# Kernel tuning notes

Hardware: AMD Instinct MI355X
Metric: run time of the kernel (lower is better)

The kernel has to match this reference:

```python
import jax, jax.numpy as jnp
import numpy as np

N = 100000       # nodes
DEG = 16         # fixed out/in degree used to build CSR
E = N * DEG      # edges
D_IN = 128       # in_feats
D_OUT = 256      # out_feats
K = 32           # maxk k_value


def _xavier_uniform(key, shape, gain):
    fan_out, fan_in = shape
    bound = gain * np.sqrt(6.0 / (fan_in + fan_out))
    return jax.random.uniform(key, shape, jnp.float32, -bound, bound)


def setup_inputs() -> dict:
    key = jax.random.key(0)
    ks = jax.random.split(key, 6)
    feat = jax.random.normal(ks[0], (N, D_IN), jnp.float32)
    topk_values = jax.random.uniform(ks[1], (N, K), jnp.float32)
    topk_indices = jax.random.randint(ks[2], (N, K), 0, D_IN).astype(jnp.int32)
    # CSR graph: fixed degree -> indptr is arange*DEG; random destinations
    indptr = (jnp.arange(N + 1) * DEG).astype(jnp.int32)
    indices = jax.random.randint(ks[3], (E,), 0, N).astype(jnp.int32)
    # set_graph_data: csr weight[e] = 1 / clamp(in_degree(dst), 1)
    in_deg = jax.ops.segment_sum(jnp.ones(E, jnp.float32), indices, num_segments=N)
    in_deg = jnp.maximum(in_deg, 1.0)
    csr_values = 1.0 / in_deg[indices]
    gain = np.sqrt(2.0)  # calculate_gain('relu')
    w_neigh = _xavier_uniform(ks[4], (D_OUT, D_IN), gain)
    w_self = _xavier_uniform(ks[5], (D_OUT, D_IN), gain)
    b_self = jnp.zeros((D_OUT,), jnp.float32)
    return {"feat": feat, "topk_values": topk_values, "csr_values": csr_values,
            "w_neigh": w_neigh, "w_self": w_self, "b_self": b_self,
            "topk_indices": topk_indices, "indptr": indptr, "indices": indices}


def reference(feat, topk_values, csr_values, w_neigh, w_self, b_self,
              topk_indices, indptr, indices):
    # Densify the k-sparse MaxK features: x[n, topk_indices[n, j]] = topk_values[n, j]
    x = jnp.zeros((N, D_IN), feat.dtype).at[
        jnp.arange(N)[:, None], topk_indices].add(topk_values)
    # Edge-weight-normalized SpMM over CSR: out[row] += w[e] * x[col[e]]
    row_ids = jnp.repeat(jnp.arange(N), jnp.diff(indptr), total_repeat_length=E)
    msgs = x[indices] * csr_values[:, None]          # [E, D_IN]
    agg = jax.ops.segment_sum(msgs, row_ids, num_segments=N)  # [N, D_IN]
    # lin_before_mp is False (in_feats <= out_feats): project after aggregation
    h_neigh = agg @ w_neigh.T                        # [N, D_OUT]
    rst = feat @ w_self.T + b_self + h_neigh         # fc_self(h_self) + h_neigh
    return rst
```

## Files before the change

kernel.cpp:

```cpp
#include <hip/hip_runtime.h>
#include <hip/hip_bf16.h>
#include <stdint.h>

#define N_NODES 100000
#define DEG 16
#define D_IN 128
#define D_OUT 256
#define K_TOP 32
#define K_CAT 256

typedef __attribute__((ext_vector_type(8))) short short8;
typedef __attribute__((ext_vector_type(4))) float floatx4;

__device__ __forceinline__ unsigned pack_bf16_rne(float f) {
    union { float f; unsigned u; } c; c.f = f;
    unsigned u = c.u;
    return (u + 0x7fffu + ((u >> 16) & 1u)) >> 16;
}
__device__ __forceinline__ float bf16lo_to_f(unsigned lo16) {
    union { unsigned u; float f; } c; c.u = lo16 << 16; return c.f;
}

__global__ __launch_bounds__(256) void k_packw(const float* __restrict__ w_self,
                                               const float* __restrict__ w_neigh,
                                               unsigned short* __restrict__ bmat) {
    int o = blockIdx.x;
    int k = threadIdx.x;
    float v = (k < D_IN) ? w_self[o * D_IN + k] : w_neigh[o * D_IN + (k - D_IN)];
    bmat[o * K_CAT + k] = (unsigned short)pack_bf16_rne(v);
}

#define DROWS 64
__global__ __launch_bounds__(256) void k_densify(const float* __restrict__ topk_v,
                                                 const int* __restrict__ topk_i,
                                                 const float* __restrict__ feat,
                                                 unsigned short* __restrict__ xbf,
                                                 unsigned short* __restrict__ abf) {
    __shared__ float sx[DROWS * D_IN];
    const int t = threadIdx.x;
    const int row0 = blockIdx.x * DROWS;

    #pragma unroll
    for (int p = 0; p < 8; ++p)
        *(floatx4*)&sx[(t + p * 256) * 4] = (floatx4){0.f, 0.f, 0.f, 0.f};
    __syncthreads();

    const size_t tbase = (size_t)row0 * K_TOP;
    #pragma unroll
    for (int p = 0; p < 8; ++p) {
        int q = t + p * 256;
        int r = q >> 5;
        if (row0 + r < N_NODES) {
            int   ci = topk_i[tbase + q];
            float cv = topk_v[tbase + q];
            atomicAdd(&sx[r * D_IN + ci], cv);
        }
    }
    __syncthreads();

    #pragma unroll
    for (int p = 0; p < 16; ++p) {
        int d = t + p * 256;
        int r = d >> 6;
        int c2 = (d & 63) * 2;
        if (row0 + r < N_NODES) {
            float2 v = *(const float2*)&sx[r * D_IN + c2];
            ((unsigned*)(xbf + (size_t)(row0 + r) * D_IN))[d & 63] =
                pack_bf16_rne(v.x) | (pack_bf16_rne(v.y) << 16);
        }
    }

    #pragma unroll
    for (int p = 0; p < 8; ++p) {
        int q = t + p * 256;
        int r = q >> 5;
        int c4 = (q & 31) * 4;
        if (row0 + r < N_NODES) {
            float4 f = *(const float4*)(feat + (size_t)(row0 + r) * D_IN + c4);
            uint2 pk;
            pk.x = pack_bf16_rne(f.x) | (pack_bf16_rne(f.y) << 16);
            pk.y = pack_bf16_rne(f.z) | (pack_bf16_rne(f.w) << 16);
            ((uint2*)(abf + (size_t)(row0 + r) * K_CAT))[q & 31] = pk;
        }
    }
}

__global__ __launch_bounds__(256) void k_spmm(const float* __restrict__ csr_w,
                                              const int* __restrict__ col_idx,
                                              const unsigned short* __restrict__ xbf,
                                              unsigned short* __restrict__ abf) {
    const int wave = threadIdx.x >> 6;
    const int lane = threadIdx.x & 63;
    const int pair = blockIdx.x * 4 + wave;
    const int row  = 2 * pair + (lane >> 5);
    const int hl   = lane & 31;
    if (row >= N_NODES) return;

    int c = 0; float w = 0.f;
    if (hl < DEG) {
        c = col_idx[row * DEG + hl];
        w = csr_w[row * DEG + hl];
    }
    const int bsel = lane & 32;
    uint2 vv[DEG];
    #pragma unroll
    for (int e = 0; e < DEG; ++e) {
        int col = __shfl(c, bsel | e);
        vv[e] = *(const uint2*)(xbf + (size_t)col * D_IN + hl * 4);
    }
    float a0 = 0.f, a1 = 0.f, a2 = 0.f, a3 = 0.f;
    #pragma unroll
    for (int e = 0; e < DEG; ++e) {
        float we = __shfl(w, bsel | e);
        a0 += we * bf16lo_to_f(vv[e].x & 0xffffu);
        a1 += we * bf16lo_to_f(vv[e].x >> 16);
        a2 += we * bf16lo_to_f(vv[e].y & 0xffffu);
        a3 += we * bf16lo_to_f(vv[e].y >> 16);
    }
    uint2 pk;
    pk.x = pack_bf16_rne(a0) | (pack_bf16_rne(a1) << 16);
    pk.y = pack_bf16_rne(a2) | (pack_bf16_rne(a3) << 16);
    ((uint2*)(abf + (size_t)row * K_CAT + D_IN))[hl] = pk;
}

#define BM 128
#define BN 256
#define BK 32
#define LDP 40

__global__ __launch_bounds__(256, 2) void k_gemm(const unsigned short* __restrict__ abf,
                                                 const unsigned short* __restrict__ bmat,
                                                 const float* __restrict__ bias,
                                                 float* __restrict__ out) {
    __shared__ unsigned short As[BM * LDP];
    __shared__ unsigned short Bs[BN * LDP];
    int t = threadIdx.x;
    int lane = t & 63, wave = t >> 6;
    int wr = wave >> 1, wc = wave & 1;
    int row0 = blockIdx.x * BM;

    floatx4 acc[4][8];
    #pragma unroll
    for (int i = 0; i < 4; ++i)
        #pragma unroll
        for (int j = 0; j < 8; ++j)
            acc[i][j] = (floatx4){0.f, 0.f, 0.f, 0.f};

    int quad = lane >> 4;
    int l16  = lane & 15;

    for (int kt = 0; kt < K_CAT; kt += BK) {
        __syncthreads();
        #pragma unroll
        for (int p = 0; p < 2; ++p) {
            int chunk = t + p * 256;
            int r  = chunk >> 2;
            int ko = (chunk & 3) * 8;
            uint4 av = make_uint4(0u, 0u, 0u, 0u);
            int gr = row0 + r;
            if (gr < N_NODES)
                av = *(const uint4*)(abf + (size_t)gr * K_CAT + kt + ko);
            *(uint4*)&As[r * LDP + ko] = av;
        }
        #pragma unroll
        for (int p = 0; p < 4; ++p) {
            int chunk = t + p * 256;
            int r  = chunk >> 2;
            int ko = (chunk & 3) * 8;
            uint4 bv = *(const uint4*)(bmat + (size_t)r * K_CAT + kt + ko);
            *(uint4*)&Bs[r * LDP + ko] = bv;
        }
        __syncthreads();

        short8 afr[4], bfr[8];
        #pragma unroll
        for (int i = 0; i < 4; ++i) {
            int m = wr * 64 + i * 16 + l16;
            afr[i] = *(const short8*)&As[m * LDP + quad * 8];
        }
        #pragma unroll
        for (int j = 0; j < 8; ++j) {
            int n = wc * 128 + j * 16 + l16;
            bfr[j] = *(const short8*)&Bs[n * LDP + quad * 8];
        }
        #pragma unroll
        for (int i = 0; i < 4; ++i)
            #pragma unroll
            for (int j = 0; j < 8; ++j)
                acc[i][j] = __builtin_amdgcn_mfma_f32_16x16x32_bf16(afr[i], bfr[j], acc[i][j], 0, 0, 0);
    }

    #pragma unroll
    for (int j = 0; j < 8; ++j) {
        int cg = wc * 128 + j * 16 + l16;
        float bv = bias[cg];
        #pragma unroll
        for (int i = 0; i < 4; ++i) {
            int mbase = row0 + wr * 64 + i * 16 + quad * 4;
            #pragma unroll
            for (int r = 0; r < 4; ++r) {
                int gr = mbase + r;
                if (gr < N_NODES) out[(size_t)gr * D_OUT + cg] = acc[i][j][r] + bv;
            }
        }
    }
}

extern "C" void kernel_launch(void* const* d_in, const int* in_sizes, int n_in,
                              void* d_out, int out_size, void* d_ws, size_t ws_size,
                              hipStream_t stream) {
    const float* feat    = (const float*)d_in[0];
    const float* topk_v  = (const float*)d_in[1];
    const float* csr_w   = (const float*)d_in[2];
    const float* w_neigh = (const float*)d_in[3];
    const float* w_self  = (const float*)d_in[4];
    const float* b_self  = (const float*)d_in[5];
    const int*   topk_i  = (const int*)d_in[6];
    const int*   indices = (const int*)d_in[8];
    float* out = (float*)d_out;

    unsigned short* xbf  = (unsigned short*)d_ws;
    unsigned short* abf  = xbf + (size_t)N_NODES * D_IN;
    unsigned short* bmat = abf + (size_t)N_NODES * K_CAT;

    k_packw<<<dim3(256), dim3(256), 0, stream>>>(w_self, w_neigh, bmat);
    k_densify<<<dim3((N_NODES + DROWS - 1) / DROWS), dim3(256), 0, stream>>>(topk_v, topk_i, feat, xbf, abf);
    k_spmm<<<dim3((N_NODES + 7) / 8), dim3(256), 0, stream>>>(csr_w, indices, xbf, abf);
    k_gemm<<<dim3((N_NODES + BM - 1) / BM), dim3(256), 0, stream>>>(abf, bmat, b_self, out);
}
```

Measured before the change: 308.2 us.

## Fuse SpMM aggregation and feat conversion into GEMM via shared-memory A tile

Merges the SpMM gather and the bf16 conversion of feat into the GEMM kernel. Each 64-row block builds its full 64x256 concatenated A tile in shared memory, then runs the MFMA loop over it while streaming only the B tiles. This drops the write and re-read of the intermediate A matrix in global memory and removes one kernel launch. In exchange the tile shrinks from 128 to 64 rows, so B is reloaded twice as often, and the gather and MFMA phases inside a block are serialized with no overlap.

```diff
diff --git a/kernel.cpp b/kernel.cpp
--- a/kernel.cpp
+++ b/kernel.cpp
@@ -33,9 +33,7 @@
 #define DROWS 64
 __global__ __launch_bounds__(256) void k_densify(const float* __restrict__ topk_v,
                                                  const int* __restrict__ topk_i,
-                                                 const float* __restrict__ feat,
-                                                 unsigned short* __restrict__ xbf,
-                                                 unsigned short* __restrict__ abf) {
+                                                 unsigned short* __restrict__ xbf) {
     __shared__ float sx[DROWS * D_IN];
     const int t = threadIdx.x;
     const int row0 = blockIdx.x * DROWS;
@@ -69,138 +67,136 @@
                 pack_bf16_rne(v.x) | (pack_bf16_rne(v.y) << 16);
         }
     }
+}
+
+#define BM 64
+#define BK 32
+#define LDA 264
+#define LDB 40
+
+__global__ __launch_bounds__(256, 3) void k_fused(const float* __restrict__ feat,
+                                                  const float* __restrict__ csr_w,
+                                                  const int* __restrict__ col_idx,
+                                                  const unsigned short* __restrict__ xbf,
+                                                  const unsigned short* __restrict__ bmat,
+                                                  const float* __restrict__ bias,
+                                                  float* __restrict__ out) {
+    __shared__ unsigned short As[BM * LDA];
+    __shared__ unsigned short Bs[D_OUT * LDB];
+    const int t = threadIdx.x;
+    const int lane = t & 63, wave = t >> 6;
+    const int row0 = blockIdx.x * BM;
+    const int quad = lane >> 4, l16 = lane & 15;
+    const int hw = t >> 5, hl = t & 31;
+
+    int   ce[8]; float we_[8];
+    #pragma unroll
+    for (int it = 0; it < 8; ++it) {
+        int gr = row0 + hw * 8 + it;
+        ce[it] = 0; we_[it] = 0.f;
+        if (hl < DEG && gr < N_NODES) {
+            ce[it] = col_idx[gr * DEG + hl];
+            we_[it] = csr_w[gr * DEG + hl];
+        }
+    }
 
     #pragma unroll
     for (int p = 0; p < 8; ++p) {
         int q = t + p * 256;
         int r = q >> 5;
         int c4 = (q & 31) * 4;
+        uint2 pk = {0u, 0u};
         if (row0 + r < N_NODES) {
             float4 f = *(const float4*)(feat + (size_t)(row0 + r) * D_IN + c4);
-            uint2 pk;
             pk.x = pack_bf16_rne(f.x) | (pack_bf16_rne(f.y) << 16);
             pk.y = pack_bf16_rne(f.z) | (pack_bf16_rne(f.w) << 16);
-            ((uint2*)(abf + (size_t)(row0 + r) * K_CAT))[q & 31] = pk;
-        }
-    }
-}
-
-__global__ __launch_bounds__(256) void k_spmm(const float* __restrict__ csr_w,
-                                              const int* __restrict__ col_idx,
-                                              const unsigned short* __restrict__ xbf,
-                                              unsigned short* __restrict__ abf) {
-    const int wave = threadIdx.x >> 6;
-    const int lane = threadIdx.x & 63;
-    const int pair = blockIdx.x * 4 + wave;
-    const int row  = 2 * pair + (lane >> 5);
-    const int hl   = lane & 31;
-    if (row >= N_NODES) return;
-
-    int c = 0; float w = 0.f;
-    if (hl < DEG) {
-        c = col_idx[row * DEG + hl];
-        w = csr_w[row * DEG + hl];
-    }
+        }
+        *(uint2*)&As[r * LDA + c4] = pk;
+    }
+
+    #pragma unroll
+    for (int p = 0; p < 4; ++p) {
+        int chunk = t + p * 256;
+        int r  = chunk >> 2;
+        int ko = (chunk & 3) * 8;
+        *(uint4*)&Bs[r * LDB + ko] = *(const uint4*)(bmat + (size_t)r * K_CAT + ko);
+    }
+
     const int bsel = lane & 32;
-    uint2 vv[DEG];
-    #pragma unroll
-    for (int e = 0; e < DEG; ++e) {
-        int col = __shfl(c, bsel | e);
-        vv[e] = *(const uint2*)(xbf + (size_t)col * D_IN + hl * 4);
-    }
-    float a0 = 0.f, a1 = 0.f, a2 = 0.f, a3 = 0.f;
-    #pragma unroll
-    for (int e = 0; e < DEG; ++e) {
-        float we = __shfl(w, bsel | e);
-        a0 += we * bf16lo_to_f(vv[e].x & 0xffffu);
-        a1 += we * bf16lo_to_f(vv[e].x >> 16);
-        a2 += we * bf16lo_to_f(vv[e].y & 0xffffu);
-        a3 += we * bf16lo_to_f(vv[e].y >> 16);
-    }
-    uint2 pk;
-    pk.x = pack_bf16_rne(a0) | (pack_bf16_rne(a1) << 16);
-    pk.y = pack_bf16_rne(a2) | (pack_bf16_rne(a3) << 16);
-    ((uint2*)(abf + (size_t)row * K_CAT + D_IN))[hl] = pk;
-}
-
-#define BM 128
-#define BN 256
-#define BK 32
-#define LDP 40
-
-__global__ __launch_bounds__(256, 2) void k_gemm(const unsigned short* __restrict__ abf,
-                                                 const unsigned short* __restrict__ bmat,
-                                                 const float* __restrict__ bias,
-                                                 float* __restrict__ out) {
-    __shared__ unsigned short As[BM * LDP];
-    __shared__ unsigned short Bs[BN * LDP];
-    int t = threadIdx.x;
-    int lane = t & 63, wave = t >> 6;
-    int wr = wave >> 1, wc = wave & 1;
-    int row0 = blockIdx.x * BM;
-
-    floatx4 acc[4][8];
+    #pragma unroll
+    for (int it = 0; it < 8; ++it) {
+        int r = hw * 8 + it;
+        uint2 vv[DEG];
+        #pragma unroll
+        for (int e = 0; e < DEG; ++e) {
+            int col = __shfl(ce[it], bsel | e);
+            vv[e] = *(const uint2*)(xbf + (size_t)col * D_IN + hl * 4);
+        }
+        float a0 = 0.f, a1 = 0.f, a2 = 0.f, a3 = 0.f;
+        #pragma unroll
+        for (int e = 0; e < DEG; ++e) {
+            float w = __shfl(we_[it], bsel | e);
+            a0 += w * bf16lo_to_f(vv[e].x & 0xffffu);
+            a1 += w * bf16lo_to_f(vv[e].x >> 16);
+            a2 += w * bf16lo_to_f(vv[e].y & 0xffffu);
+            a3 += w * bf16lo_to_f(vv[e].y >> 16);
+        }
+        uint2 pk;
+        pk.x = pack_bf16_rne(a0) | (pack_bf16_rne(a1) << 16);
+        pk.y = pack_bf16_rne(a2) | (pack_bf16_rne(a3) << 16);
+        *(uint2*)&As[r * LDA + D_IN + hl * 4] = pk;
+    }
+
+    floatx4 acc[4][4];
     #pragma unroll
     for (int i = 0; i < 4; ++i)
         #pragma unroll
-        for (int j = 0; j < 8; ++j)
+        for (int j = 0; j < 4; ++j)
             acc[i][j] = (floatx4){0.f, 0.f, 0.f, 0.f};
 
-    int quad = lane >> 4;
-    int l16  = lane & 15;
+    __syncthreads();
 
     for (int kt = 0; kt < K_CAT; kt += BK) {
-        __syncthreads();
-        #pragma unroll
-        for (int p = 0; p < 2; ++p) {
-            int chunk = t + p * 256;
-            int r  = chunk >> 2;
-            int ko = (chunk & 3) * 8;
-            uint4 av = make_uint4(0u, 0u, 0u, 0u);
-            int gr = row0 + r;
-            if (gr < N_NODES)
-                av = *(const uint4*)(abf + (size_t)gr * K_CAT + kt + ko);
-            *(uint4*)&As[r * LDP + ko] = av;
-        }
-        #pragma unroll
-        for (int p = 0; p < 4; ++p) {
-            int chunk = t + p * 256;
-            int r  = chunk >> 2;
-            int ko = (chunk & 3) * 8;
-            uint4 bv = *(const uint4*)(bmat + (size_t)r * K_CAT + kt + ko);
-            *(uint4*)&Bs[r * LDP + ko] = bv;
-        }
-        __syncthreads();
-
-        short8 afr[4], bfr[8];
+        if (kt) {
+            __syncthreads();
+            #pragma unroll
+            for (int p = 0; p < 4; ++p) {
+                int chunk = t + p * 256;
+                int r  = chunk >> 2;
+                int ko = (chunk & 3) * 8;
+                *(uint4*)&Bs[r * LDB + ko] = *(const uint4*)(bmat + (size_t)r * K_CAT + kt + ko);
+            }
+            __syncthreads();
+        }
+        short8 afr[4], bfr[4];
         #pragma unroll
         for (int i = 0; i < 4; ++i) {
-            int m = wr * 64 + i * 16 + l16;
-            afr[i] = *(const short8*)&As[m * LDP + quad * 8];
-        }
-        #pragma unroll
-        for (int j = 0; j < 8; ++j) {
-            int n = wc * 128 + j * 16 + l16;
-            bfr[j] = *(const short8*)&Bs[n * LDP + quad * 8];
+            int m = i * 16 + l16;
+            afr[i] = *(const short8*)&As[m * LDA + kt + quad * 8];
+        }
+        #pragma unroll
+        for (int j = 0; j < 4; ++j) {
+            int n = wave * 64 + j * 16 + l16;
+            bfr[j] = *(const short8*)&Bs[n * LDB + quad * 8];
         }
         #pragma unroll
         for (int i = 0; i < 4; ++i)
             #pragma unroll
-            for (int j = 0; j < 8; ++j)
+            for (int j = 0; j < 4; ++j)
                 acc[i][j] = __builtin_amdgcn_mfma_f32_16x16x32_bf16(afr[i], bfr[j], acc[i][j], 0, 0, 0);
     }
 
     #pragma unroll
-    for (int j = 0; j < 8; ++j) {
-        int cg = wc * 128 + j * 16 + l16;
+    for (int j = 0; j < 4; ++j) {
+        int cg = wave * 64 + j * 16 + l16;
         float bv = bias[cg];
         #pragma unroll
         for (int i = 0; i < 4; ++i) {
-            int mbase = row0 + wr * 64 + i * 16 + quad * 4;
+            int mbase = row0 + i * 16 + quad * 4;
             #pragma unroll
-            for (int r = 0; r < 4; ++r) {
-                int gr = mbase + r;
-                if (gr < N_NODES) out[(size_t)gr * D_OUT + cg] = acc[i][j][r] + bv;
+            for (int rr = 0; rr < 4; ++rr) {
+                int gr = mbase + rr;
+                if (gr < N_NODES) out[(size_t)gr * D_OUT + cg] = acc[i][j][rr] + bv;
             }
         }
     }
@@ -220,11 +216,9 @@
     float* out = (float*)d_out;
 
     unsigned short* xbf  = (unsigned short*)d_ws;
-    unsigned short* abf  = xbf + (size_t)N_NODES * D_IN;
-    unsigned short* bmat = abf + (size_t)N_NODES * K_CAT;
+    unsigned short* bmat = xbf + (size_t)N_NODES * D_IN;
 
     k_packw<<<dim3(256), dim3(256), 0, stream>>>(w_self, w_neigh, bmat);
-    k_densify<<<dim3((N_NODES + DROWS - 1) / DROWS), dim3(256), 0, stream>>>(topk_v, topk_i, feat, xbf, abf);
-    k_spmm<<<dim3((N_NODES + 7) / 8), dim3(256), 0, stream>>>(csr_w, indices, xbf, abf);
-    k_gemm<<<dim3((N_NODES + BM - 1) / BM), dim3(256), 0, stream>>>(abf, bmat, b_self, out);
-}
+    k_densify<<<dim3((N_NODES + DROWS - 1) / DROWS), dim3(256), 0, stream>>>(topk_v, topk_i, xbf);
+    k_fused<<<dim3((N_NODES + BM - 1) / BM), dim3(256), 0, stream>>>(feat, csr_w, indices, xbf, bmat, b_self, out);
+}
```

Measured after the change: 308.8 us. Within noise of the previous version (+0.2%).
